# Kernel tuning notes

Measured on AMD Instinct MI355X. Metric: run time of the kernel, lower is better.

## Reference

```python
import jax, jax.numpy as jnp
import numpy as np

N = 60000   # cells
F = 256     # CELL_FEATURE_DIM
H = 128     # HIDDEN_DIM
NH = 8      # NUM_HEADS
DH = H // NH
L = 2       # NUM_LAYERS
C = 256     # tissue clusters
E = 600000  # cell edges
ET = 1500   # tissue edges
NCLS = 4


def _seg_softmax(s, seg, n):
    # numerically stable softmax within segments; s: [E, NH]
    m = jax.ops.segment_max(s, seg, num_segments=n)
    e = jnp.exp(s - m[seg])
    z = jax.ops.segment_sum(e, seg, num_segments=n)
    return e / z[seg]


def _forward(cell_features, cluster_labels, cell_edge_index, tissue_edge_index,
             W_cell_proj, b_cell_proj, W_tissue_proj, b_tissue_proj,
             gat_W, gat_asrc, gat_adst, gat_b, gcn_W, gcn_b,
             bu_Wq, bu_Wk, bu_Wv, bu_bq, bu_bk, bu_bv, bu_Wo, bu_bo,
             td_Wv, td_bv, td_Wo, td_bo,
             gru_Wih, gru_bih, gru_Whh, gru_bhh,
             Wc1, bc1, Wc2, bc2, Wc3, bc3):
    lab = cluster_labels
    # tissue node init = per-cluster mean of raw cell features (as in _construct_tissue_graph)
    cnt = jax.ops.segment_sum(jnp.ones((N,), jnp.float32), lab, num_segments=C)
    tissue_x = jax.ops.segment_sum(cell_features, lab, num_segments=C) / jnp.maximum(cnt, 1.0)[:, None]

    cell_h = cell_features @ W_cell_proj.T + b_cell_proj      # [N, H]
    tissue_h = tissue_x @ W_tissue_proj.T + b_tissue_proj     # [C, H]

    # add self-loops (PyG GATConv / GCNConv default)
    csrc = jnp.concatenate([cell_edge_index[0], jnp.arange(N, dtype=cell_edge_index.dtype)])
    cdst = jnp.concatenate([cell_edge_index[1], jnp.arange(N, dtype=cell_edge_index.dtype)])
    tsrc = jnp.concatenate([tissue_edge_index[0], jnp.arange(C, dtype=tissue_edge_index.dtype)])
    tdst = jnp.concatenate([tissue_edge_index[1], jnp.arange(C, dtype=tissue_edge_index.dtype)])

    # GCN symmetric norm (deg over col, PyG gcn_norm)
    degc = jax.ops.segment_sum(jnp.ones_like(tdst, dtype=jnp.float32), tdst, num_segments=C)
    dinv = jnp.where(degc > 0, 1.0 / jnp.sqrt(degc), 0.0)
    w_e = (dinv[tsrc] * dinv[tdst])[:, None]

    scale = 1.0 / jnp.sqrt(jnp.float32(DH))

    for l in range(L):
        # --- GATConv (multi-head concat) + ELU ---
        h = (cell_h @ gat_W[l].T).reshape(N, NH, DH)
        a_s = (h * gat_asrc[l]).sum(-1)  # [N, NH]
        a_d = (h * gat_adst[l]).sum(-1)
        e = jax.nn.leaky_relu(a_s[csrc] + a_d[cdst], negative_slope=0.2)  # [E+N, NH]
        alpha = _seg_softmax(e, cdst, N)
        agg = jax.ops.segment_sum(h[csrc] * alpha[:, :, None], cdst, num_segments=N)
        cell_h = jax.nn.elu(agg.reshape(N, H) + gat_b[l])

        # --- GCNConv + ReLU on tissue graph ---
        th = tissue_h @ gcn_W[l].T
        tissue_h = jax.nn.relu(jax.ops.segment_sum(th[tsrc] * w_e, tdst, num_segments=C) + gcn_b[l])

        # --- bottom-up cross-level attention: tissue queries attend over their cells ---
        q = ((tissue_h @ bu_Wq.T + bu_bq) * scale).reshape(C, NH, DH)
        k = (cell_h @ bu_Wk.T + bu_bk).reshape(N, NH, DH)
        v = (cell_h @ bu_Wv.T + bu_bv).reshape(N, NH, DH)
        s_att = (q[lab] * k).sum(-1)                       # [N, NH]
        al = _seg_softmax(s_att, lab, C)
        ctx = jax.ops.segment_sum(v * al[:, :, None], lab, num_segments=C).reshape(C, H)
        tissue_h = ctx @ bu_Wo.T + bu_bo

        # --- top-down attention: each cell attends to its single tissue node ---
        # softmax over one key is identically 1, so output = Wo(Wv t + bv) + bo gathered per cell
        td = (tissue_h @ td_Wv.T + td_bv) @ td_Wo.T + td_bo  # [C, H]
        cell_h = td[lab]

        # --- top-down GRUCell refinement: x=[cell;tissue], h=cell ---
        x_in = jnp.concatenate([cell_h, tissue_h[lab]], axis=-1)  # [N, 2H]
        gi = x_in @ gru_Wih.T + gru_bih
        gh = cell_h @ gru_Whh.T + gru_bhh
        r = jax.nn.sigmoid(gi[:, :H] + gh[:, :H])
        z = jax.nn.sigmoid(gi[:, H:2 * H] + gh[:, H:2 * H])
        n = jnp.tanh(gi[:, 2 * H:] + r * gh[:, 2 * H:])
        cell_h = (1.0 - z) * n + z * cell_h

    # dual-pooling readouts (single graph: batch all zeros)
    emb = jnp.concatenate([cell_h.mean(0), cell_h.max(0), tissue_h.mean(0), tissue_h.max(0)])[None, :]  # [1, 4H]
    h1 = jax.nn.relu(emb @ Wc1.T + bc1)
    h2 = jax.nn.relu(h1 @ Wc2.T + bc2)
    return h2 @ Wc3.T + bc3  # [1, NCLS]


def setup_inputs() -> dict:
    k = jax.random.split(jax.random.key(0), 40)
    s = 0.05
    r = lambda i, shape: jax.random.normal(k[i], shape, jnp.float32) * s
    return dict(
        cell_features=jax.random.normal(k[0], (N, F), jnp.float32),
        cell_edge_index=jax.random.randint(k[1], (2, E), 0, N),
        cluster_labels=jax.random.randint(k[2], (N,), 0, C),
        tissue_edge_index=jax.random.randint(k[3], (2, ET), 0, C),
        W_cell_proj=r(4, (H, F)), b_cell_proj=r(5, (H,)),
        W_tissue_proj=r(6, (H, F)), b_tissue_proj=r(7, (H,)),
        gat_W=r(8, (L, H, H)), gat_asrc=r(9, (L, NH, DH)), gat_adst=r(10, (L, NH, DH)), gat_b=r(11, (L, H)),
        gcn_W=r(12, (L, H, H)), gcn_b=r(13, (L, H)),
        bu_Wq=r(14, (H, H)), bu_Wk=r(15, (H, H)), bu_Wv=r(16, (H, H)),
        bu_bq=r(17, (H,)), bu_bk=r(18, (H,)), bu_bv=r(19, (H,)),
        bu_Wo=r(20, (H, H)), bu_bo=r(21, (H,)),
        td_Wv=r(22, (H, H)), td_bv=r(23, (H,)), td_Wo=r(24, (H, H)), td_bo=r(25, (H,)),
        gru_Wih=r(26, (3 * H, 2 * H)), gru_bih=r(27, (3 * H,)),
        gru_Whh=r(28, (3 * H, H)), gru_bhh=r(29, (3 * H,)),
        Wc1=r(30, (2 * H, 4 * H)), bc1=r(31, (2 * H,)),
        Wc2=r(32, (H, 2 * H)), bc2=r(33, (H,)),
        Wc3=r(34, (NCLS, H)), bc3=r(35, (NCLS,)),
    )


def reference(cell_features, cell_edge_index, cluster_labels, tissue_edge_index,
              W_cell_proj, b_cell_proj, W_tissue_proj, b_tissue_proj,
              gat_W, gat_asrc, gat_adst, gat_b, gcn_W, gcn_b,
              bu_Wq, bu_Wk, bu_Wv, bu_bq, bu_bk, bu_bv, bu_Wo, bu_bo,
              td_Wv, td_bv, td_Wo, td_bo,
              gru_Wih, gru_bih, gru_Whh, gru_bhh,
              Wc1, bc1, Wc2, bc2, Wc3, bc3):
    return _forward(cell_features, cluster_labels, cell_edge_index, tissue_edge_index,
                    W_cell_proj, b_cell_proj, W_tissue_proj, b_tissue_proj,
                    gat_W, gat_asrc, gat_adst, gat_b, gcn_W, gcn_b,
                    bu_Wq, bu_Wk, bu_Wv, bu_bq, bu_bk, bu_bv, bu_Wo, bu_bo,
                    td_Wv, td_bv, td_Wo, td_bo,
                    gru_Wih, gru_bih, gru_Whh, gru_bhh,
                    Wc1, bc1, Wc2, bc2, Wc3, bc3)
```

## Files before the change

### kernel.cpp

```cpp
#include <hip/hip_runtime.h>
#include <math.h>

constexpr int N  = 60000;
constexpr int F  = 256;
constexpr int H  = 128;
constexpr int C  = 256;
constexpr int E  = 600000;
constexpr int ET = 1500;
constexpr int NB = (N + 1023) / 1024;
constexpr int SPL = 8;
constexpr int PB  = 16;

typedef __attribute__((ext_vector_type(8))) short short8;
typedef __attribute__((ext_vector_type(4))) float f32x4;

__device__ __forceinline__ unsigned short f2b(float f) {
  unsigned int u = __float_as_uint(f);
  return (unsigned short)((u + 0x7FFFu + ((u >> 16) & 1u)) >> 16);
}
__device__ __forceinline__ float b2f(unsigned short b) {
  return __uint_as_float(((unsigned int)b) << 16);
}

__global__ void hg_hist(const int* __restrict__ cdst, int* __restrict__ deg,
                        const int* __restrict__ lab, int* __restrict__ ccnt) {
  int e = blockIdx.x * 256 + threadIdx.x;
  if (e < E) atomicAdd(&deg[cdst[e]], 1);
  if (e < N) atomicAdd(&ccnt[lab[e]], 1);
}

__global__ __launch_bounds__(256) void hg_scan1(const int* __restrict__ deg, int* __restrict__ off,
                                                int* __restrict__ btot, int n) {
  int b = blockIdx.x, t = threadIdx.x;
  int i0 = b * 1024 + t * 4;
  __shared__ int sums[256];
  int d0 = 0, d1 = 0, d2 = 0, d3 = 0;
  if (i0 + 3 < n) {
    int4 dd = *(const int4*)&deg[i0];
    d0 = dd.x; d1 = dd.y; d2 = dd.z; d3 = dd.w;
  } else {
    if (i0     < n) d0 = deg[i0];
    if (i0 + 1 < n) d1 = deg[i0 + 1];
    if (i0 + 2 < n) d2 = deg[i0 + 2];
    if (i0 + 3 < n) d3 = deg[i0 + 3];
  }
  int s = d0 + d1 + d2 + d3;
  sums[t] = s;
  __syncthreads();
  for (int ofs = 1; ofs < 256; ofs <<= 1) {
    int v = (t >= ofs) ? sums[t - ofs] : 0;
    __syncthreads();
    sums[t] += v;
    __syncthreads();
  }
  int excl = sums[t] - s;
  if (t == 255) btot[b] = sums[t];
  int run = excl;
  if (i0     < n) off[i0]     = run; run += d0;
  if (i0 + 1 < n) off[i0 + 1] = run; run += d1;
  if (i0 + 2 < n) off[i0 + 2] = run; run += d2;
  if (i0 + 3 < n) off[i0 + 3] = run;
}

__global__ __launch_bounds__(256) void hg_scan2_setup(int* __restrict__ btot, int* __restrict__ off,
                                                      const int* __restrict__ ccnt, int* __restrict__ coff,
                                                      const int* __restrict__ tsrc, const int* __restrict__ tdst,
                                                      int* __restrict__ toff, int* __restrict__ tlist,
                                                      float* __restrict__ dinv) {
  __shared__ int sa[256], sb[256], sc2[256];
  int t = threadIdx.x;
  if (blockIdx.x == 0) {
    if (t < 64) sa[t] = (t < NB) ? btot[t] : 0;
    __syncthreads();
    if (t == 0) {
      int r = 0;
      for (int i = 0; i < NB; ++i) { int v = sa[i]; sa[i] = r; r += v; }
      off[N] = r;
    }
    __syncthreads();
    if (t < NB) btot[t] = sa[t];
  } else if (blockIdx.x == 1) {
    int v0 = ccnt[t];
    sa[t] = v0;
    __syncthreads();
    for (int ofs = 1; ofs < 256; ofs <<= 1) {
      int v = (t >= ofs) ? sa[t - ofs] : 0;
      __syncthreads();
      sa[t] += v;
      __syncthreads();
    }
    coff[t + 1] = sa[t];
    if (t == 0) coff[0] = 0;
  } else {
    sa[t] = 0;
    __syncthreads();
    for (int e = t; e < ET; e += 256) atomicAdd(&sa[tdst[e]], 1);
    __syncthreads();
    int v = sa[t];
    dinv[t] = rsqrtf((float)(v + 1));
    sb[t] = v;
    __syncthreads();
    for (int ofs = 1; ofs < 256; ofs <<= 1) {
      int u = (t >= ofs) ? sb[t - ofs] : 0;
      __syncthreads();
      sb[t] += u;
      __syncthreads();
    }
    toff[t + 1] = sb[t];
    if (t == 0) toff[0] = 0;
    sc2[t] = sb[t] - v;
    __syncthreads();
    for (int e = t; e < ET; e += 256) {
      int d = tdst[e];
      int p = atomicAdd(&sc2[d], 1);
      tlist[p] = tsrc[e];
    }
  }
}

__global__ void hg_scan3(int* __restrict__ off, const int* __restrict__ btot, int n) {
  int b = blockIdx.x;
  int addv = btot[b];
  int i0 = b * 1024 + threadIdx.x * 4;
#pragma unroll
  for (int r = 0; r < 4; ++r)
    if (i0 + r < n) off[i0 + r] += addv;
}

__global__ void hg_scatter(const int* __restrict__ csrc, const int* __restrict__ cdst,
                           const int* __restrict__ off, int* __restrict__ cur, int* __restrict__ csr,
                           const int* __restrict__ lab, const int* __restrict__ coff,
                           int* __restrict__ ccur, int* __restrict__ list) {
  int e = blockIdx.x * 256 + threadIdx.x;
  if (e < E) {
    int d = cdst[e];
    int p = atomicAdd(&cur[d], 1);
    csr[off[d] + p] = csrc[e];
  }
  if (e < N) {
    int c = lab[e];
    int p = atomicAdd(&ccur[c], 1);
    list[coff[c] + p] = e;
  }
}

struct TJob { const float* src; float* dst; int SR; int SC; int dld; };
struct PrepArgs {
  TJob j[8];
  const float* gatW1; const float* Wcp; const float* bcp; short* Wcompb; float* bcomp;
  const float* tdWo; const float* tdWv; const float* tdbv; const float* tdbo;
  float* A_td; float* Wcat_t; float* bcat;
};

__global__ __launch_bounds__(256) void hg_prep1(PrepArgs a) {
  int y = blockIdx.y, t = threadIdx.x;
  if (y < 8) {
    TJob jb = a.j[y];
    int total = jb.SR * jb.SC;
    for (int idx = blockIdx.x * 256 + t; idx < total; idx += gridDim.x * 256) {
      int r = idx / jb.SC, c = idx - r * jb.SC;
      jb.dst[(size_t)c * jb.dld + r] = jb.src[idx];
    }
  } else if (y == 8) {
    int j = blockIdx.x, k = t;
    float acc = 0.f;
#pragma unroll 4
    for (int m = 0; m < 128; ++m) acc = fmaf(a.gatW1[j * 128 + m], a.Wcp[m * 256 + k], acc);
    a.Wcompb[(size_t)j * 256 + k] = (short)f2b(acc);
    if (k == 0) {
      float b = 0.f;
      for (int m = 0; m < 128; ++m) b = fmaf(a.gatW1[j * 128 + m], a.bcp[m], b);
      a.bcomp[j] = b;
    }
  } else if (blockIdx.x < 64) {
    int j = blockIdx.x * 2 + (t >> 7), k = t & 127;
    float acc = 0.f;
#pragma unroll 4
    for (int p = 0; p < 128; ++p) acc = fmaf(a.tdWo[j * 128 + p], a.tdWv[p * 128 + k], acc);
    a.A_td[j * 128 + k] = acc;
    a.Wcat_t[k * 896 + j] = acc;
    if (k == 0) {
      float b = 0.f;
      for (int p = 0; p < 128; ++p) b = fmaf(a.tdWo[j * 128 + p], a.tdbv[p], b);
      a.bcat[j] = b + a.tdbo[j];
    }
  }
}

__global__ __launch_bounds__(256) void hg_pc2b(const float* __restrict__ Wih, const float* __restrict__ bih,
                                               const float* __restrict__ Whh, const float* __restrict__ bhh,
                                               const float* __restrict__ A_td, float* __restrict__ Wcat_t,
                                               float* __restrict__ bcat) {
  int jj = blockIdx.x * 2 + (threadIdx.x >> 7), k = threadIdx.x & 127;
  const float* coef;
  float extra, bb;
  int dcol, j;
  if (jj < 384) {
    j = jj; coef = Wih + (size_t)j * 256; extra = Wih[(size_t)j * 256 + 128 + k]; dcol = 128 + j; bb = bih[j];
  } else {
    j = jj - 384; coef = Whh + (size_t)j * 128; extra = 0.f; dcol = 512 + j; bb = bhh[j];
  }
  float a = 0.f;
#pragma unroll 4
  for (int m = 0; m < 128; ++m) a = fmaf(coef[m], A_td[m * 128 + k], a);
  Wcat_t[k * 896 + dcol] = a + extra;
  if (k == 0) {
    float b = 0.f;
    for (int m = 0; m < 128; ++m) b = fmaf(coef[m], bcat[m], b);
    bcat[dcol] = b + bb;
  }
}

__global__ __launch_bounds__(256, 2) void hg_gemm_coef(
    const float* __restrict__ A, int M, int rtiles,
    const short* __restrict__ Wb,
    const float* __restrict__ bias,
    unsigned short* __restrict__ outp,
    const float* __restrict__ avs, const float* __restrict__ avd,
    float* __restrict__ o_s, float* __restrict__ o_d,
    const int* __restrict__ list, const int* __restrict__ coff,
    const float* __restrict__ Wtpt, const float* __restrict__ btp, float* __restrict__ tish) {
  __shared__ float mrow[256];
  const int t = threadIdx.x;

  if (blockIdx.x >= rtiles) {
    int c = blockIdx.x - rtiles;
    int s0 = coff[c], n = coff[c + 1] - s0;
    float acc = 0.f;
#pragma unroll 4
    for (int i = 0; i < n; ++i) acc += A[(size_t)list[s0 + i] * F + t];
    mrow[t] = acc / fmaxf((float)n, 1.f);
    __syncthreads();
    if (t < 128) {
      float a = btp[t];
#pragma unroll 4
      for (int k = 0; k < 256; ++k) a = fmaf(mrow[k], Wtpt[k * 128 + t], a);
      tish[c * 128 + t] = a;
    }
    return;
  }

  const int w = t >> 6, l = t & 63;
  const int li = l & 15, lk = l >> 4;
  const int m0 = blockIdx.x * 128 + w * 32;

  f32x4 zero = {0.f, 0.f, 0.f, 0.f};
  f32x4 acc[2][8];
#pragma unroll
  for (int rt = 0; rt < 2; ++rt)
#pragma unroll
    for (int ct = 0; ct < 8; ++ct) acc[rt][ct] = zero;

  const int r0 = m0 + li, r1 = m0 + 16 + li;
  const bool v0 = r0 < M, v1 = r1 < M;
  const float* a0p = A + (size_t)r0 * 256 + lk * 8;
  const float* a1p = A + (size_t)r1 * 256 + lk * 8;

  for (int kc = 0; kc < 256; kc += 32) {
    short8 bf[8];
#pragma unroll
    for (int ct = 0; ct < 8; ++ct)
      bf[ct] = *(const short8*)&Wb[(size_t)(ct * 16 + li) * 256 + kc + lk * 8];
    short8 af0 = {0, 0, 0, 0, 0, 0, 0, 0};
    short8 af1 = {0, 0, 0, 0, 0, 0, 0, 0};
    if (v0) {
      float4 x = *(const float4*)(a0p + kc);
      float4 y = *(const float4*)(a0p + kc + 4);
      af0[0] = (short)f2b(x.x); af0[1] = (short)f2b(x.y); af0[2] = (short)f2b(x.z); af0[3] = (short)f2b(x.w);
      af0[4] = (short)f2b(y.x); af0[5] = (short)f2b(y.y); af0[6] = (short)f2b(y.z); af0[7] = (short)f2b(y.w);
    }
    if (v1) {
      float4 x = *(const float4*)(a1p + kc);
      float4 y = *(const float4*)(a1p + kc + 4);
      af1[0] = (short)f2b(x.x); af1[1] = (short)f2b(x.y); af1[2] = (short)f2b(x.z); af1[3] = (short)f2b(x.w);
      af1[4] = (short)f2b(y.x); af1[5] = (short)f2b(y.y); af1[6] = (short)f2b(y.z); af1[7] = (short)f2b(y.w);
    }
#pragma unroll
    for (int ct = 0; ct < 8; ++ct) {
      acc[0][ct] = __builtin_amdgcn_mfma_f32_16x16x32_bf16(af0, bf[ct], acc[0][ct], 0, 0, 0);
      acc[1][ct] = __builtin_amdgcn_mfma_f32_16x16x32_bf16(af1, bf[ct], acc[1][ct], 0, 0, 0);
    }
  }

#pragma unroll
  for (int ct = 0; ct < 8; ++ct) {
    float bj = bias[ct * 16 + li];
    float as = avs[ct * 16 + li];
    float ad = avd[ct * 16 + li];
#pragma unroll
    for (int rt = 0; rt < 2; ++rt) {
#pragma unroll
      for (int r = 0; r < 4; ++r) {
        int gm = m0 + rt * 16 + lk * 4 + r;
        float v = acc[rt][ct][r] + bj;
        if (gm < M) outp[(size_t)gm * 128 + ct * 16 + li] = f2b(v);
        float ps = v * as, pd = v * ad;
        ps += __shfl_xor(ps, 1); ps += __shfl_xor(ps, 2); ps += __shfl_xor(ps, 4); ps += __shfl_xor(ps, 8);
        pd += __shfl_xor(pd, 1); pd += __shfl_xor(pd, 2); pd += __shfl_xor(pd, 4); pd += __shfl_xor(pd, 8);
        if (li == 0 && gm < M) {
          o_s[(size_t)gm * 8 + ct] = ps;
          o_d[(size_t)gm * 8 + ct] = pd;
        }
      }
    }
  }
}

#define GMAXE 64
__global__ __launch_bounds__(256) void hg_gat_agg(
    const unsigned short* __restrict__ hproj, const float* __restrict__ a_s,
    const float* __restrict__ a_d, const int* __restrict__ remap,
    const int* __restrict__ off, const int* __restrict__ csr,
    const float* __restrict__ bias, unsigned short* __restrict__ outh,
    const float* __restrict__ qk, const float* __restrict__ qb,
    const int* __restrict__ lab, const int* __restrict__ nodelist,
    float* __restrict__ satt, int nNodes) {
  const int wid = threadIdx.x >> 6;
  const int l = threadIdx.x & 63;
  const int gid = blockIdx.x * 4 + wid;
  __shared__ int srcs_s[4][GMAXE];
  __shared__ float w_s[4][GMAXE][8];
  if (gid >= nNodes) return;
  const int node = nodelist[gid];
  int* srcs = srcs_s[wid];
  float (*wls)[8] = w_s[wid];
  const int o0 = off[node], deg = off[node + 1] - o0;
  const int cl = lab[node];
  const int dl = remap ? cl : node;
  const int hsc = l & 7;
  const int q4 = l & 31;
  const int sub = l >> 5;
  const int hq = q4 >> 2;
  const float adh = a_d[dl * 8 + hsc];
  const float ash = a_s[dl * 8 + hsc];
  float msc = -INFINITY, zsc = 0.f;
  float4 acc = make_float4(0.f, 0.f, 0.f, 0.f);
  const ushort4* hp4 = (const ushort4*)hproj;

  for (int cb = 0; cb < deg; cb += GMAXE) {
    const int len = min(GMAXE, deg - cb);
    if (l < len) {
      int s = csr[o0 + cb + l];
      srcs[l] = remap ? remap[s] : s;
    }
    asm volatile("s_waitcnt lgkmcnt(0)" ::: "memory");
    float lm = -INFINITY;
    for (int base = 0; base < len; base += 8) {
      int e = base + (l >> 3);
      if (e < len) {
        float sc = a_s[srcs[e] * 8 + hsc] + adh;
        sc = sc > 0.f ? sc : 0.2f * sc;
        wls[e][hsc] = sc;
        lm = fmaxf(lm, sc);
      }
    }
    lm = fmaxf(lm, __shfl_xor(lm, 8));
    lm = fmaxf(lm, __shfl_xor(lm, 16));
    lm = fmaxf(lm, __shfl_xor(lm, 32));
    float mnew = fmaxf(msc, lm);
    float rs = __expf(msc - mnew);
    float zc = 0.f;
    asm volatile("s_waitcnt lgkmcnt(0)" ::: "memory");
    for (int base = 0; base < len; base += 8) {
      int e = base + (l >> 3);
      if (e < len) {
        float wv = __expf(wls[e][hsc] - mnew);
        wls[e][hsc] = wv;
        zc += wv;
      }
    }
    asm volatile("s_waitcnt lgkmcnt(0)" ::: "memory");
    zc += __shfl_xor(zc, 8); zc += __shfl_xor(zc, 16); zc += __shfl_xor(zc, 32);
    zsc = zsc * rs + zc;
    msc = mnew;
    float rsa = __shfl(rs, hq);
    acc.x *= rsa; acc.y *= rsa; acc.z *= rsa; acc.w *= rsa;
    for (int e = sub; e < len; e += 2) {
      float wv = wls[e][hq];
      ushort4 hv = hp4[(size_t)srcs[e] * 32 + q4];
      acc.x = fmaf(wv, b2f(hv.x), acc.x);
      acc.y = fmaf(wv, b2f(hv.y), acc.y);
      acc.z = fmaf(wv, b2f(hv.z), acc.z);
      acc.w = fmaf(wv, b2f(hv.w), acc.w);
    }
  }
  float ssl = ash + adh;
  ssl = ssl > 0.f ? ssl : 0.2f * ssl;
  float mnew = fmaxf(msc, ssl);
  float rs = __expf(msc - mnew);
  float wsl = __expf(ssl - mnew);
  zsc = zsc * rs + wsl;
  float rsa = __shfl(rs, hq);
  float wsa = __shfl(wsl, hq);
  float zh = __shfl(zsc, hq);
  acc.x *= rsa; acc.y *= rsa; acc.z *= rsa; acc.w *= rsa;
  acc.x += __shfl_xor(acc.x, 32);
  acc.y += __shfl_xor(acc.y, 32);
  acc.z += __shfl_xor(acc.z, 32);
  acc.w += __shfl_xor(acc.w, 32);
  ushort4 hvs = hp4[(size_t)dl * 32 + q4];
  acc.x = fmaf(wsa, b2f(hvs.x), acc.x);
  acc.y = fmaf(wsa, b2f(hvs.y), acc.y);
  acc.z = fmaf(wsa, b2f(hvs.z), acc.z);
  acc.w = fmaf(wsa, b2f(hvs.w), acc.w);
  float inv = 1.f / zh;
  float4 bv4 = *(const float4*)&bias[q4 * 4];
  float4 o;
  o.x = acc.x * inv + bv4.x;
  o.y = acc.y * inv + bv4.y;
  o.z = acc.z * inv + bv4.z;
  o.w = acc.w * inv + bv4.w;
  o.x = o.x > 0.f ? o.x : __expf(o.x) - 1.f;
  o.y = o.y > 0.f ? o.y : __expf(o.y) - 1.f;
  o.z = o.z > 0.f ? o.z : __expf(o.z) - 1.f;
  o.w = o.w > 0.f ? o.w : __expf(o.w) - 1.f;
  if (sub == 0) {
    ushort4 ov = make_ushort4(f2b(o.x), f2b(o.y), f2b(o.z), f2b(o.w));
    ((ushort4*)outh)[(size_t)node * 32 + q4] = ov;
  }

  const float4* qk4 = (const float4*)(qk + (size_t)cl * 1024);
  float p0, p1, p2, p3;
  {
    float4 qv0 = qk4[(sub * 4 + 0) * 32 + q4];
    float4 qv1 = qk4[(sub * 4 + 1) * 32 + q4];
    float4 qv2 = qk4[(sub * 4 + 2) * 32 + q4];
    float4 qv3 = qk4[(sub * 4 + 3) * 32 + q4];
    p0 = o.x * qv0.x + o.y * qv0.y + o.z * qv0.z + o.w * qv0.w;
    p1 = o.x * qv1.x + o.y * qv1.y + o.z * qv1.z + o.w * qv1.w;
    p2 = o.x * qv2.x + o.y * qv2.y + o.z * qv2.z + o.w * qv2.w;
    p3 = o.x * qv3.x + o.y * qv3.y + o.z * qv3.z + o.w * qv3.w;
  }
  int b4f = (l >> 4) & 1, b3f = (l >> 3) & 1;
  float snd0 = b4f ? p0 : p2, snd1 = b4f ? p1 : p3;
  float kp0  = b4f ? p2 : p0, kp1  = b4f ? p3 : p1;
  kp0 += __shfl_xor(snd0, 16);
  kp1 += __shfl_xor(snd1, 16);
  float snd = b3f ? kp0 : kp1;
  float kp  = b3f ? kp1 : kp0;
  kp += __shfl_xor(snd, 8);
  kp += __shfl_xor(kp, 4);
  kp += __shfl_xor(kp, 2);
  kp += __shfl_xor(kp, 1);
  int h = sub * 4 + b4f * 2 + b3f;
  if ((l & 7) == 0) satt[(size_t)node * 8 + h] = kp + qb[cl * 8 + h];
}

__global__ __launch_bounds__(128) void hg_gcn_q(const float* __restrict__ tin, const int* __restrict__ toff,
                                                const int* __restrict__ tlist, const float* __restrict__ dinv,
                                                const float* __restrict__ gt, const float* __restrict__ gcnb,
                                                const float* __restrict__ Wqt, const float* __restrict__ bq,
                                                const float* __restrict__ Wk, const float* __restrict__ bk,
                                                float* __restrict__ qk, float* __restrict__ qb) {
  int c = blockIdx.x, t = threadIdx.x;
  __shared__ float xa[128], trow[128], qrow[128];
  float dc = dinv[c];
  float acc = tin[c * 128 + t] * dc * dc;
  int s0 = toff[c], s1 = toff[c + 1];
  for (int i = s0; i < s1; ++i) {
    int s = tlist[i];
    acc = fmaf(tin[s * 128 + t], dinv[s] * dc, acc);
  }
  xa[t] = acc;
  __syncthreads();
  float th = 0.f;
#pragma unroll 4
  for (int k = 0; k < 128; ++k) th = fmaf(xa[k], gt[k * 128 + t], th);
  float vv = fmaxf(th + gcnb[t], 0.f);
  trow[t] = vv;
  __syncthreads();
  float qa = bq[t];
#pragma unroll 4
  for (int k = 0; k < 128; ++k) qa = fmaf(trow[k], Wqt[k * 128 + t], qa);
  qrow[t] = qa * 0.25f;
  __syncthreads();
#pragma unroll
  for (int h = 0; h < 8; ++h) {
    float s = 0.f;
#pragma unroll
    for (int j = 0; j < 16; ++j) s = fmaf(Wk[(size_t)(h * 16 + j) * 128 + t], qrow[h * 16 + j], s);
    qk[((size_t)c * 8 + h) * 128 + t] = s;
  }
  if (t < 8) {
    float s = 0.f;
#pragma unroll
    for (int j = 0; j < 16; ++j) s = fmaf(qrow[t * 16 + j], bk[t * 16 + j], s);
    qb[c * 8 + t] = s;
  }
}

__global__ __launch_bounds__(256) void hg_bu_part(
    const float* __restrict__ s_att, const unsigned short* __restrict__ hcell,
    const int* __restrict__ list, const int* __restrict__ coff,
    float* __restrict__ pm, float* __restrict__ pz, float* __restrict__ pmacc) {
  int c = blockIdx.x, sp = blockIdx.y, t = threadIdx.x;
  int s0 = coff[c], n = coff[c + 1] - s0;
  int chunk = (n + SPL - 1) / SPL;
  int b0 = min(n, sp * chunk), b1 = min(n, b0 + chunk);
  int cnt = b1 - b0;
  int tf = t & 127, half = t >> 7;
  __shared__ float red[32][8];
  __shared__ float mh[8];
  __shared__ int cells[64];
  __shared__ float wl[64][8];
  __shared__ float msh[8][128];
  int g = t >> 3, h8 = t & 7;
  float lm = -INFINITY;
  for (int i = g; i < cnt; i += 32) lm = fmaxf(lm, s_att[(size_t)list[s0 + b0 + i] * 8 + h8]);
  red[g][h8] = lm;
  __syncthreads();
  if (t < 8) {
    float m2 = -INFINITY;
#pragma unroll
    for (int i = 0; i < 32; ++i) m2 = fmaxf(m2, red[i][t]);
    mh[t] = m2;
  }
  __syncthreads();
  const float mloc = mh[t & 7];
  float zp = 0.f;
  float macc[8] = {0.f, 0.f, 0.f, 0.f, 0.f, 0.f, 0.f, 0.f};
  for (int cb = 0; cb < cnt; cb += 64) {
    int len = min(64, cnt - cb);
    if (t < len) cells[t] = list[s0 + b0 + cb + t];
    __syncthreads();
#pragma unroll
    for (int p = 0; p < 2; ++p) {
      int e = p * 32 + (t >> 3);
      if (e < len) {
        float w = __expf(s_att[(size_t)cells[e] * 8 + (t & 7)] - mloc);
        wl[e][t & 7] = w;
        zp += w;
      }
    }
    __syncthreads();
    for (int e = half; e < len; e += 2) {
      float x = b2f(hcell[(size_t)cells[e] * 128 + tf]);
      float4 w0 = *(const float4*)&wl[e][0];
      float4 w1 = *(const float4*)&wl[e][4];
      macc[0] = fmaf(w0.x, x, macc[0]);
      macc[1] = fmaf(w0.y, x, macc[1]);
      macc[2] = fmaf(w0.z, x, macc[2]);
      macc[3] = fmaf(w0.w, x, macc[3]);
      macc[4] = fmaf(w1.x, x, macc[4]);
      macc[5] = fmaf(w1.y, x, macc[5]);
      macc[6] = fmaf(w1.z, x, macc[6]);
      macc[7] = fmaf(w1.w, x, macc[7]);
    }
    __syncthreads();
  }
  red[t >> 3][t & 7] = zp;
  __syncthreads();
  int pidx = (c * SPL + sp) * 8;
  if (t < 8) {
    float z = 0.f;
#pragma unroll
    for (int i = 0; i < 32; ++i) z += red[i][t];
    pz[pidx + t] = z;
    pm[pidx + t] = mh[t];
  }
  if (half) {
#pragma unroll
    for (int h = 0; h < 8; ++h) msh[h][tf] = macc[h];
  }
  __syncthreads();
  if (!half) {
#pragma unroll
    for (int h = 0; h < 8; ++h) pmacc[(size_t)(pidx + h) * 128 + tf] = macc[h] + msh[h][tf];
  }
}

__global__ __launch_bounds__(256) void hg_bu_chain(
    const float* __restrict__ pm, const float* __restrict__ pz, const float* __restrict__ pmacc,
    const float* __restrict__ Wv, const float* __restrict__ bv,
    const float* __restrict__ Wot, const float* __restrict__ bo,
    const float* __restrict__ Wcat_t, const float* __restrict__ bcat,
    const float* __restrict__ gatWt, const float* __restrict__ avs, const float* __restrict__ avd,
    float* __restrict__ tish, float* __restrict__ ccell,
    unsigned short* __restrict__ hprojc, float* __restrict__ a_s2, float* __restrict__ a_d2) {
  int c = blockIdx.x, t = threadIdx.x;
  int tf = t & 127, half = t >> 7;
  __shared__ float mh[8], zh[8];
  __shared__ float sscale[SPL][8];
  __shared__ float msh[8][128];
  __shared__ float b0[128], b1[128], part[2][128], catv[896];
  const int pbase = c * SPL * 8;
  if (t < 8) {
    float mg = -INFINITY;
#pragma unroll
    for (int s = 0; s < SPL; ++s) mg = fmaxf(mg, pm[pbase + s * 8 + t]);
    mh[t] = mg;
  }
  __syncthreads();
  if (t < SPL * 8) {
    int s = t >> 3, h = t & 7;
    float ms = pm[pbase + s * 8 + h];
    sscale[s][h] = (ms > -1e37f) ? __expf(ms - mh[h]) : 0.f;
  }
  __syncthreads();
  if (t < 8) {
    float z = 0.f;
#pragma unroll
    for (int s = 0; s < SPL; ++s) z += pz[pbase + s * 8 + t] * sscale[s][t];
    zh[t] = (z > 0.f) ? 1.f / z : 0.f;
  }
  __syncthreads();
#pragma unroll
  for (int hh = 0; hh < 4; ++hh) {
    int h = half * 4 + hh;
    float a = 0.f;
#pragma unroll
    for (int s = 0; s < SPL; ++s)
      a = fmaf(pmacc[(size_t)(pbase + s * 8 + h) * 128 + tf], sscale[s][h], a);
    msh[h][tf] = a * zh[h];
  }
  __syncthreads();
  {
    int h = tf >> 4;
    float ps = 0.f;
    const float* wp = Wv + (size_t)tf * 128 + half * 64;
    const float* mp = &msh[h][half * 64];
#pragma unroll 4
    for (int k = 0; k < 64; ++k) ps = fmaf(wp[k], mp[k], ps);
    part[half][tf] = ps;
  }
  __syncthreads();
  if (t < 128) b0[t] = part[0][t] + part[1][t] + bv[t];
  __syncthreads();
  int ks = half;
  {
    float ps = 0.f;
    const float* wp = Wot + (size_t)ks * 64 * 128 + tf;
#pragma unroll 4
    for (int k = 0; k < 64; ++k) ps = fmaf(b0[ks * 64 + k], wp[k * 128], ps);
    part[ks][tf] = ps;
  }
  __syncthreads();
  if (t < 128) {
    float vv = part[0][t] + part[1][t] + bo[t];
    b1[t] = vv;
    tish[c * 128 + t] = vv;
  }
  __syncthreads();
  for (int j = t; j < 896; j += 256) {
    float a = bcat[j];
#pragma unroll 4
    for (int k = 0; k < 128; ++k) a = fmaf(b1[k], Wcat_t[k * 896 + j], a);
    catv[j] = a;
  }
  __syncthreads();
  if (t < 128) {
    float td = catv[t];
    float r = 1.f / (1.f + expf(-(catv[128 + t] + catv[512 + t])));
    float zz = 1.f / (1.f + expf(-(catv[256 + t] + catv[640 + t])));
    float nn = tanhf(catv[384 + t] + r * catv[768 + t]);
    float cn = (1.f - zz) * nn + zz * td;
    ccell[c * 128 + t] = cn;
    b0[t] = cn;
  }
  __syncthreads();
  if (gatWt) {
    float ps = 0.f;
    const float* wp = gatWt + (size_t)ks * 64 * 128 + tf;
#pragma unroll 4
    for (int k = 0; k < 64; ++k) ps = fmaf(b0[ks * 64 + k], wp[k * 128], ps);
    part[ks][tf] = ps;
    __syncthreads();
    if (t < 128) {
      float hp = part[0][t] + part[1][t];
      hprojc[c * 128 + t] = f2b(hp);
      float pss = hp * avs[t], pdd = hp * avd[t];
      pss += __shfl_xor(pss, 1); pss += __shfl_xor(pss, 2); pss += __shfl_xor(pss, 4); pss += __shfl_xor(pss, 8);
      pdd += __shfl_xor(pdd, 1); pdd += __shfl_xor(pdd, 2); pdd += __shfl_xor(pdd, 4); pdd += __shfl_xor(pdd, 8);
      if ((t & 15) == 0) {
        a_s2[c * 8 + (t >> 4)] = pss;
        a_d2[c * 8 + (t >> 4)] = pdd;
      }
    }
  }
}

__global__ __launch_bounds__(256) void hg_pool(const float* __restrict__ ccell2, const float* __restrict__ tish,
                                               const int* __restrict__ cnt, float* __restrict__ part) {
  int b = blockIdx.x, t = threadIdx.x;
  int c0 = b * (C / PB);
  if (t < 128) {
    float sm = 0.f, mx = -INFINITY;
#pragma unroll 4
    for (int i = 0; i < C / PB; ++i) {
      int c = c0 + i;
      float vv = ccell2[c * 128 + t];
      int n = cnt[c];
      sm += (float)n * vv;
      if (n > 0) mx = fmaxf(mx, vv);
    }
    part[b * 512 + t] = sm;
    part[b * 512 + 128 + t] = mx;
  } else {
    int tt = t - 128;
    float sm = 0.f, mx = -INFINITY;
#pragma unroll 4
    for (int i = 0; i < C / PB; ++i) {
      int c = c0 + i;
      float vv = tish[c * 128 + tt];
      sm += vv;
      mx = fmaxf(mx, vv);
    }
    part[b * 512 + 256 + tt] = sm;
    part[b * 512 + 384 + tt] = mx;
  }
}

__global__ __launch_bounds__(256) void hg_mlp(const float* __restrict__ part, const float* __restrict__ Wc1t,
                                              const float* __restrict__ bc1, const float* __restrict__ Wc2t,
                                              const float* __restrict__ bc2, const float* __restrict__ Wc3,
                                              const float* __restrict__ bc3, float* __restrict__ outp) {
  __shared__ float emb[512], h1s[256], h2s[128];
  int t = threadIdx.x;
  if (t < 128) {
    float sm = 0.f, mx = -INFINITY;
#pragma unroll
    for (int b = 0; b < PB; ++b) {
      sm += part[b * 512 + t];
      mx = fmaxf(mx, part[b * 512 + 128 + t]);
    }
    emb[t] = sm / (float)N;
    emb[128 + t] = mx;
  } else {
    int tt = t - 128;
    float sm = 0.f, mx = -INFINITY;
#pragma unroll
    for (int b = 0; b < PB; ++b) {
      sm += part[b * 512 + 256 + tt];
      mx = fmaxf(mx, part[b * 512 + 384 + tt]);
    }
    emb[256 + tt] = sm * (1.f / (float)C);
    emb[384 + tt] = mx;
  }
  __syncthreads();
  float a = bc1[t];
#pragma unroll 4
  for (int kk = 0; kk < 512; ++kk) a = fmaf(emb[kk], Wc1t[kk * 256 + t], a);
  h1s[t] = fmaxf(a, 0.f);
  __syncthreads();
  if (t < 128) {
    float a2 = bc2[t];
#pragma unroll 4
    for (int kk = 0; kk < 256; ++kk) a2 = fmaf(h1s[kk], Wc2t[kk * 128 + t], a2);
    h2s[t] = fmaxf(a2, 0.f);
  }
  __syncthreads();
  if (t < 4) {
    float o = bc3[t];
    for (int kk = 0; kk < 128; ++kk) o = fmaf(h2s[kk], Wc3[t * 128 + kk], o);
    outp[t] = o;
  }
}

extern "C" void kernel_launch(void* const* d_in, const int* in_sizes, int n_in,
                              void* d_out, int out_size, void* d_ws, size_t ws_size,
                              hipStream_t stream) {
  (void)in_sizes; (void)n_in; (void)out_size; (void)ws_size;
  const float* feat  = (const float*)d_in[0];
  const int*   eidx  = (const int*)d_in[1];
  const int*   lab   = (const int*)d_in[2];
  const int*   tidx  = (const int*)d_in[3];
  const float* Wcp   = (const float*)d_in[4];
  const float* bcp   = (const float*)d_in[5];
  const float* Wtp   = (const float*)d_in[6];
  const float* btp   = (const float*)d_in[7];
  const float* gatW  = (const float*)d_in[8];
  const float* gasrc = (const float*)d_in[9];
  const float* gadst = (const float*)d_in[10];
  const float* gatb  = (const float*)d_in[11];
  const float* gcnW  = (const float*)d_in[12];
  const float* gcnb  = (const float*)d_in[13];
  const float* buWq  = (const float*)d_in[14];
  const float* buWk  = (const float*)d_in[15];
  const float* buWv  = (const float*)d_in[16];
  const float* bubq  = (const float*)d_in[17];
  const float* bubk  = (const float*)d_in[18];
  const float* bubv  = (const float*)d_in[19];
  const float* buWo  = (const float*)d_in[20];
  const float* bubo  = (const float*)d_in[21];
  const float* tdWv  = (const float*)d_in[22];
  const float* tdbv  = (const float*)d_in[23];
  const float* tdWo  = (const float*)d_in[24];
  const float* tdbo  = (const float*)d_in[25];
  const float* Wih   = (const float*)d_in[26];
  const float* bih   = (const float*)d_in[27];
  const float* Whh   = (const float*)d_in[28];
  const float* bhh   = (const float*)d_in[29];
  const float* Wc1   = (const float*)d_in[30];
  const float* bc1   = (const float*)d_in[31];
  const float* Wc2   = (const float*)d_in[32];
  const float* bc2   = (const float*)d_in[33];
  const float* Wc3   = (const float*)d_in[34];
  const float* bc3   = (const float*)d_in[35];
  float* outp = (float*)d_out;

  const int* csrc = eidx;
  const int* cdst = eidx + E;
  const int* tsrc = tidx;
  const int* tdst = tidx + ET;

  char* w = (char*)d_ws;
  auto alloc = [&](size_t bytes) -> void* {
    void* p = (void*)w;
    w += (bytes + 255) & ~(size_t)255;
    return p;
  };
  char* cnt0 = w;
  int* deg_cell = (int*)alloc((size_t)N * 4);
  int* cur_cell = (int*)alloc((size_t)N * 4);
  int* clu_cnt  = (int*)alloc((size_t)C * 4);
  int* clu_cur  = (int*)alloc((size_t)C * 4);
  size_t cntBytes = (size_t)(w - cnt0);
  int* off_cell = (int*)alloc((size_t)(N + 1) * 4);
  int* btot     = (int*)alloc(64 * 4);
  int* csr      = (int*)alloc((size_t)E * 4);
  int* clu_off  = (int*)alloc((size_t)(C + 1) * 4);
  int* clu_list = (int*)alloc((size_t)N * 4);
  int* toff     = (int*)alloc((size_t)(C + 1) * 4);
  int* tlist    = (int*)alloc((size_t)ET * 4);
  float* dinv   = (float*)alloc((size_t)C * 4);
  unsigned short* buf1 = (unsigned short*)alloc((size_t)N * 128 * 2);
  unsigned short* buf2 = (unsigned short*)alloc((size_t)N * 128 * 2);
  float* a_s    = (float*)alloc((size_t)N * 8 * 4);
  float* a_d    = (float*)alloc((size_t)N * 8 * 4);
  float* s_att  = (float*)alloc((size_t)N * 8 * 4);
  float* tish   = (float*)alloc((size_t)C * 128 * 4);
  float* qkb    = (float*)alloc((size_t)C * 8 * 128 * 4);
  float* qbb    = (float*)alloc((size_t)C * 8 * 4);
  float* ccell  = (float*)alloc((size_t)C * 128 * 4);
  unsigned short* hprojc = (unsigned short*)alloc((size_t)C * 128 * 2);
  float* a_sc   = (float*)alloc((size_t)C * 8 * 4);
  float* a_dc   = (float*)alloc((size_t)C * 8 * 4);
  float* pm     = (float*)alloc((size_t)C * SPL * 8 * 4);
  float* pz     = (float*)alloc((size_t)C * SPL * 8 * 4);
  float* pmacc  = (float*)alloc((size_t)C * SPL * 8 * 128 * 4);
  float* poolp  = (float*)alloc((size_t)PB * 512 * 4);
  float* A_td   = (float*)alloc(128 * 128 * 4);
  float* Wcat_t = (float*)alloc(128 * 896 * 4);
  float* bcat   = (float*)alloc(896 * 4);
  short* Wcompb = (short*)alloc(128 * 256 * 2);
  float* bcomp  = (float*)alloc(128 * 4);
  float* Wtpt   = (float*)alloc(256 * 128 * 4);
  float* g1t    = (float*)alloc(128 * 128 * 4);
  float* g2t    = (float*)alloc(128 * 128 * 4);
  float* Wqt    = (float*)alloc(128 * 128 * 4);
  float* Wot    = (float*)alloc(128 * 128 * 4);
  float* gatW2t = (float*)alloc(128 * 128 * 4);
  float* Wc1t   = (float*)alloc(512 * 256 * 4);
  float* Wc2t   = (float*)alloc(256 * 128 * 4);

  hipMemsetAsync(cnt0, 0, cntBytes, stream);

  hg_hist<<<(E + 255) / 256, 256, 0, stream>>>(cdst, deg_cell, lab, clu_cnt);
  hg_scan1<<<NB, 256, 0, stream>>>(deg_cell, off_cell, btot, N);
  hg_scan2_setup<<<3, 256, 0, stream>>>(btot, off_cell, clu_cnt, clu_off, tsrc, tdst, toff, tlist, dinv);
  hg_scan3<<<NB, 256, 0, stream>>>(off_cell, btot, N);
  hg_scatter<<<(E + 255) / 256, 256, 0, stream>>>(csrc, cdst, off_cell, cur_cell, csr,
                                                  lab, clu_off, clu_cur, clu_list);

  PrepArgs pa;
  pa.j[0] = {Wtp,            Wtpt,   128, 256, 128};
  pa.j[1] = {gcnW,           g1t,    128, 128, 128};
  pa.j[2] = {gcnW + 128*128, g2t,    128, 128, 128};
  pa.j[3] = {buWq,           Wqt,    128, 128, 128};
  pa.j[4] = {buWo,           Wot,    128, 128, 128};
  pa.j[5] = {gatW + 128*128, gatW2t, 128, 128, 128};
  pa.j[6] = {Wc1,            Wc1t,   256, 512, 256};
  pa.j[7] = {Wc2,            Wc2t,   128, 256, 128};
  pa.gatW1 = gatW; pa.Wcp = Wcp; pa.bcp = bcp; pa.Wcompb = Wcompb; pa.bcomp = bcomp;
  pa.tdWo = tdWo; pa.tdWv = tdWv; pa.tdbv = tdbv; pa.tdbo = tdbo;
  pa.A_td = A_td; pa.Wcat_t = Wcat_t; pa.bcat = bcat;
  hg_prep1<<<dim3(128, 10), 256, 0, stream>>>(pa);
  hg_pc2b<<<384, 256, 0, stream>>>(Wih, bih, Whh, bhh, A_td, Wcat_t, bcat);

  const int RT = (N + 127) / 128;
  hg_gemm_coef<<<RT + C, 256, 0, stream>>>(feat, N, RT, Wcompb, bcomp, buf2, gasrc, gadst, a_s, a_d,
                                           clu_list, clu_off, Wtpt, btp, tish);
  hg_gcn_q<<<C, 128, 0, stream>>>(tish, toff, tlist, dinv, g1t, gcnb, Wqt, bubq, buWk, bubk, qkb, qbb);
  hg_gat_agg<<<(N + 3) / 4, 256, 0, stream>>>(buf2, a_s, a_d, nullptr, off_cell, csr, gatb, buf1,
                                              qkb, qbb, lab, clu_list, s_att, N);
  hg_bu_part<<<dim3(C, SPL), 256, 0, stream>>>(s_att, buf1, clu_list, clu_off, pm, pz, pmacc);
  hg_bu_chain<<<C, 256, 0, stream>>>(pm, pz, pmacc, buWv, bubv, Wot, bubo, Wcat_t, bcat,
                                     gatW2t, gasrc + 128, gadst + 128, tish, ccell, hprojc, a_sc, a_dc);
  hg_gcn_q<<<C, 128, 0, stream>>>(tish, toff, tlist, dinv, g2t, gcnb + 128, Wqt, bubq, buWk, bubk, qkb, qbb);
  hg_gat_agg<<<(N + 3) / 4, 256, 0, stream>>>(hprojc, a_sc, a_dc, lab, off_cell, csr, gatb + 128, buf1,
                                              qkb, qbb, lab, clu_list, s_att, N);
  hg_bu_part<<<dim3(C, SPL), 256, 0, stream>>>(s_att, buf1, clu_list, clu_off, pm, pz, pmacc);
  hg_bu_chain<<<C, 256, 0, stream>>>(pm, pz, pmacc, buWv, bubv, Wot, bubo, Wcat_t, bcat,
                                     nullptr, nullptr, nullptr, tish, ccell, nullptr, nullptr, nullptr);

  hg_pool<<<PB, 256, 0, stream>>>(ccell, tish, clu_cnt, poolp);
  hg_mlp<<<1, 256, 0, stream>>>(poolp, Wc1t, bc1, Wc2t, bc2, Wc3, bc3, outp);
}
```

Measured before the change: 546.0 us.

## Fold GAT attention vectors into GEMM weights and tabulate layer-2 cluster attention

```diff
diff --git a/kernel.cpp b/kernel.cpp
--- a/kernel.cpp
+++ b/kernel.cpp
@@ -150,6 +150,7 @@
   const float* gatW1; const float* Wcp; const float* bcp; short* Wcompb; float* bcomp;
   const float* tdWo; const float* tdWv; const float* tdbv; const float* tdbo;
   float* A_td; float* Wcat_t; float* bcat;
+  const float* avs; const float* avd; float* sbias;
 };
 
 __global__ __launch_bounds__(256) void hg_prep1(PrepArgs a) {
@@ -172,7 +173,8 @@
       for (int m = 0; m < 128; ++m) b = fmaf(a.gatW1[j * 128 + m], a.bcp[m], b);
       a.bcomp[j] = b;
     }
-  } else if (blockIdx.x < 64) {
+  } else if (y == 9) {
+    if (blockIdx.x >= 64) return;
     int j = blockIdx.x * 2 + (t >> 7), k = t & 127;
     float acc = 0.f;
 #pragma unroll 4
@@ -183,6 +185,27 @@
       float b = 0.f;
       for (int p = 0; p < 128; ++p) b = fmaf(a.tdWo[j * 128 + p], a.tdbv[p], b);
       a.bcat[j] = b + a.tdbo[j];
+    }
+  } else {
+    if (blockIdx.x >= 16) return;
+    __shared__ float u[128];
+    int dir = blockIdx.x >> 3, h = blockIdx.x & 7;
+    const float* av = (dir == 0 ? a.avs : a.avd) + h * 16;
+    if (t < 128) {
+      float s = 0.f;
+#pragma unroll
+      for (int j = 0; j < 16; ++j) s = fmaf(a.gatW1[(size_t)(h * 16 + j) * 128 + t], av[j], s);
+      u[t] = s;
+    }
+    __syncthreads();
+    float q = 0.f;
+#pragma unroll 4
+    for (int m = 0; m < 128; ++m) q = fmaf(u[m], a.Wcp[m * 256 + t], q);
+    a.Wcompb[(size_t)(128 + dir * 8 + h) * 256 + t] = (short)f2b(q);
+    if (t == 0) {
+      float cs = 0.f;
+      for (int m = 0; m < 128; ++m) cs = fmaf(u[m], a.bcp[m], cs);
+      a.sbias[dir * 8 + h] = cs;
     }
   }
 }
@@ -211,13 +234,13 @@
   }
 }
 
-__global__ __launch_bounds__(256, 2) void hg_gemm_coef(
+__global__ __launch_bounds__(256, 3) void hg_gemm_coef(
     const float* __restrict__ A, int M, int rtiles,
     const short* __restrict__ Wb,
     const float* __restrict__ bias,
+    const float* __restrict__ sbias,
     unsigned short* __restrict__ outp,
-    const float* __restrict__ avs, const float* __restrict__ avd,
-    float* __restrict__ o_s, float* __restrict__ o_d,
+    float* __restrict__ ab,
     const int* __restrict__ list, const int* __restrict__ coff,
     const float* __restrict__ Wtpt, const float* __restrict__ btp, float* __restrict__ tish) {
   __shared__ float mrow[256];
@@ -245,11 +268,11 @@
   const int m0 = blockIdx.x * 128 + w * 32;
 
   f32x4 zero = {0.f, 0.f, 0.f, 0.f};
-  f32x4 acc[2][8];
+  f32x4 acc[2][9];
 #pragma unroll
   for (int rt = 0; rt < 2; ++rt)
 #pragma unroll
-    for (int ct = 0; ct < 8; ++ct) acc[rt][ct] = zero;
+    for (int ct = 0; ct < 9; ++ct) acc[rt][ct] = zero;
 
   const int r0 = m0 + li, r1 = m0 + 16 + li;
   const bool v0 = r0 < M, v1 = r1 < M;
@@ -257,9 +280,9 @@
   const float* a1p = A + (size_t)r1 * 256 + lk * 8;
 
   for (int kc = 0; kc < 256; kc += 32) {
-    short8 bf[8];
-#pragma unroll
-    for (int ct = 0; ct < 8; ++ct)
+    short8 bf[9];
+#pragma unroll
+    for (int ct = 0; ct < 9; ++ct)
       bf[ct] = *(const short8*)&Wb[(size_t)(ct * 16 + li) * 256 + kc + lk * 8];
     short8 af0 = {0, 0, 0, 0, 0, 0, 0, 0};
     short8 af1 = {0, 0, 0, 0, 0, 0, 0, 0};
@@ -276,7 +299,7 @@
       af1[4] = (short)f2b(y.x); af1[5] = (short)f2b(y.y); af1[6] = (short)f2b(y.z); af1[7] = (short)f2b(y.w);
     }
 #pragma unroll
-    for (int ct = 0; ct < 8; ++ct) {
+    for (int ct = 0; ct < 9; ++ct) {
       acc[0][ct] = __builtin_amdgcn_mfma_f32_16x16x32_bf16(af0, bf[ct], acc[0][ct], 0, 0, 0);
       acc[1][ct] = __builtin_amdgcn_mfma_f32_16x16x32_bf16(af1, bf[ct], acc[1][ct], 0, 0, 0);
     }
@@ -285,22 +308,23 @@
 #pragma unroll
   for (int ct = 0; ct < 8; ++ct) {
     float bj = bias[ct * 16 + li];
-    float as = avs[ct * 16 + li];
-    float ad = avd[ct * 16 + li];
 #pragma unroll
     for (int rt = 0; rt < 2; ++rt) {
 #pragma unroll
       for (int r = 0; r < 4; ++r) {
         int gm = m0 + rt * 16 + lk * 4 + r;
-        float v = acc[rt][ct][r] + bj;
-        if (gm < M) outp[(size_t)gm * 128 + ct * 16 + li] = f2b(v);
-        float ps = v * as, pd = v * ad;
-        ps += __shfl_xor(ps, 1); ps += __shfl_xor(ps, 2); ps += __shfl_xor(ps, 4); ps += __shfl_xor(ps, 8);
-        pd += __shfl_xor(pd, 1); pd += __shfl_xor(pd, 2); pd += __shfl_xor(pd, 4); pd += __shfl_xor(pd, 8);
-        if (li == 0 && gm < M) {
-          o_s[(size_t)gm * 8 + ct] = ps;
-          o_d[(size_t)gm * 8 + ct] = pd;
-        }
+        if (gm < M) outp[(size_t)gm * 128 + ct * 16 + li] = f2b(acc[rt][ct][r] + bj);
+      }
+    }
+  }
+  {
+    float sb = sbias[li];
+#pragma unroll
+    for (int rt = 0; rt < 2; ++rt) {
+#pragma unroll
+      for (int r = 0; r < 4; ++r) {
+        int gm = m0 + rt * 16 + lk * 4 + r;
+        if (gm < M) ab[(size_t)gm * 16 + li] = acc[rt][8][r] + sb;
       }
     }
   }
@@ -308,8 +332,7 @@
 
 #define GMAXE 64
 __global__ __launch_bounds__(256) void hg_gat_agg(
-    const unsigned short* __restrict__ hproj, const float* __restrict__ a_s,
-    const float* __restrict__ a_d, const int* __restrict__ remap,
+    const unsigned short* __restrict__ hproj, const float* __restrict__ ab,
     const int* __restrict__ off, const int* __restrict__ csr,
     const float* __restrict__ bias, unsigned short* __restrict__ outh,
     const float* __restrict__ qk, const float* __restrict__ qb,
@@ -326,29 +349,25 @@
   float (*wls)[8] = w_s[wid];
   const int o0 = off[node], deg = off[node + 1] - o0;
   const int cl = lab[node];
-  const int dl = remap ? cl : node;
   const int hsc = l & 7;
   const int q4 = l & 31;
   const int sub = l >> 5;
   const int hq = q4 >> 2;
-  const float adh = a_d[dl * 8 + hsc];
-  const float ash = a_s[dl * 8 + hsc];
+  const float adh = ab[(size_t)node * 16 + 8 + hsc];
+  const float ash = ab[(size_t)node * 16 + hsc];
   float msc = -INFINITY, zsc = 0.f;
   float4 acc = make_float4(0.f, 0.f, 0.f, 0.f);
   const ushort4* hp4 = (const ushort4*)hproj;
 
   for (int cb = 0; cb < deg; cb += GMAXE) {
     const int len = min(GMAXE, deg - cb);
-    if (l < len) {
-      int s = csr[o0 + cb + l];
-      srcs[l] = remap ? remap[s] : s;
-    }
+    if (l < len) srcs[l] = csr[o0 + cb + l];
     asm volatile("s_waitcnt lgkmcnt(0)" ::: "memory");
     float lm = -INFINITY;
     for (int base = 0; base < len; base += 8) {
       int e = base + (l >> 3);
       if (e < len) {
-        float sc = a_s[srcs[e] * 8 + hsc] + adh;
+        float sc = ab[(size_t)srcs[e] * 16 + hsc] + adh;
         sc = sc > 0.f ? sc : 0.2f * sc;
         wls[e][hsc] = sc;
         lm = fmaxf(lm, sc);
@@ -398,7 +417,7 @@
   acc.y += __shfl_xor(acc.y, 32);
   acc.z += __shfl_xor(acc.z, 32);
   acc.w += __shfl_xor(acc.w, 32);
-  ushort4 hvs = hp4[(size_t)dl * 32 + q4];
+  ushort4 hvs = hp4[(size_t)node * 32 + q4];
   acc.x = fmaf(wsa, b2f(hvs.x), acc.x);
   acc.y = fmaf(wsa, b2f(hvs.y), acc.y);
   acc.z = fmaf(wsa, b2f(hvs.z), acc.z);
@@ -444,6 +463,129 @@
   kp += __shfl_xor(kp, 1);
   int h = sub * 4 + b4f * 2 + b3f;
   if ((l & 7) == 0) satt[(size_t)node * 8 + h] = kp + qb[cl * 8 + h];
+}
+
+__global__ __launch_bounds__(256) void hg_ttab(const float* __restrict__ a_sc, const float* __restrict__ a_dc,
+                                               float* __restrict__ T) {
+  int cd = blockIdx.x, cs = threadIdx.x;
+  __shared__ float as[256][8];
+  __shared__ float mx[8];
+#pragma unroll
+  for (int h = 0; h < 8; ++h) as[cs][h] = a_sc[cs * 8 + h];
+  __syncthreads();
+  if (cs < 8) {
+    float m = -INFINITY;
+    for (int i = 0; i < 256; ++i) m = fmaxf(m, as[i][cs]);
+    mx[cs] = m;
+  }
+  __syncthreads();
+  float* Trow = T + ((size_t)cd * 256 + cs) * 8;
+#pragma unroll
+  for (int h = 0; h < 8; ++h) {
+    float ad = a_dc[cd * 8 + h];
+    float s = as[cs][h] + ad;
+    s = s > 0.f ? s : 0.2f * s;
+    float sm = mx[h] + ad;
+    sm = sm > 0.f ? sm : 0.2f * sm;
+    Trow[h] = __expf(s - sm);
+  }
+}
+
+__global__ __launch_bounds__(256) void hg_gat_agg2(
+    const unsigned short* __restrict__ hproj,
+    const float* __restrict__ T,
+    const int* __restrict__ lab, const int* __restrict__ off, const int* __restrict__ csr,
+    const float* __restrict__ bias, unsigned short* __restrict__ outh,
+    const float* __restrict__ qk, const float* __restrict__ qb,
+    const int* __restrict__ nodelist, float* __restrict__ satt, int nNodes) {
+  const int wid = threadIdx.x >> 6;
+  const int l = threadIdx.x & 63;
+  const int gid = blockIdx.x * 4 + wid;
+  __shared__ int srcs_s[4][GMAXE];
+  if (gid >= nNodes) return;
+  const int node = nodelist[gid];
+  int* srcs = srcs_s[wid];
+  const int o0 = off[node], deg = off[node + 1] - o0;
+  const int cd = lab[node];
+  const int q4 = l & 31;
+  const int sub = l >> 5;
+  const int hq = q4 >> 2;
+  const float* Trow = T + (size_t)cd * 2048;
+  const ushort4* hp4 = (const ushort4*)hproj;
+  float4 acc = make_float4(0.f, 0.f, 0.f, 0.f);
+  float z = 0.f;
+
+  for (int cb = 0; cb < deg; cb += GMAXE) {
+    const int len = min(GMAXE, deg - cb);
+    if (l < len) srcs[l] = lab[csr[o0 + cb + l]];
+    asm volatile("s_waitcnt lgkmcnt(0)" ::: "memory");
+    for (int e = sub; e < len; e += 2) {
+      int cs = srcs[e];
+      float tw = Trow[cs * 8 + hq];
+      ushort4 hv = hp4[(size_t)cs * 32 + q4];
+      acc.x = fmaf(tw, b2f(hv.x), acc.x);
+      acc.y = fmaf(tw, b2f(hv.y), acc.y);
+      acc.z = fmaf(tw, b2f(hv.z), acc.z);
+      acc.w = fmaf(tw, b2f(hv.w), acc.w);
+      z += tw;
+    }
+    asm volatile("s_waitcnt lgkmcnt(0)" ::: "memory");
+  }
+  acc.x += __shfl_xor(acc.x, 32);
+  acc.y += __shfl_xor(acc.y, 32);
+  acc.z += __shfl_xor(acc.z, 32);
+  acc.w += __shfl_xor(acc.w, 32);
+  z += __shfl_xor(z, 32);
+  {
+    float tw = Trow[cd * 8 + hq];
+    ushort4 hv = hp4[(size_t)cd * 32 + q4];
+    acc.x = fmaf(tw, b2f(hv.x), acc.x);
+    acc.y = fmaf(tw, b2f(hv.y), acc.y);
+    acc.z = fmaf(tw, b2f(hv.z), acc.z);
+    acc.w = fmaf(tw, b2f(hv.w), acc.w);
+    z += tw;
+  }
+  float inv = 1.f / z;
+  float4 bv4 = *(const float4*)&bias[q4 * 4];
+  float4 o;
+  o.x = acc.x * inv + bv4.x;
+  o.y = acc.y * inv + bv4.y;
+  o.z = acc.z * inv + bv4.z;
+  o.w = acc.w * inv + bv4.w;
+  o.x = o.x > 0.f ? o.x : __expf(o.x) - 1.f;
+  o.y = o.y > 0.f ? o.y : __expf(o.y) - 1.f;
+  o.z = o.z > 0.f ? o.z : __expf(o.z) - 1.f;
+  o.w = o.w > 0.f ? o.w : __expf(o.w) - 1.f;
+  if (sub == 0) {
+    ushort4 ov = make_ushort4(f2b(o.x), f2b(o.y), f2b(o.z), f2b(o.w));
+    ((ushort4*)outh)[(size_t)node * 32 + q4] = ov;
+  }
+
+  const float4* qk4 = (const float4*)(qk + (size_t)cd * 1024);
+  float p0, p1, p2, p3;
+  {
+    float4 qv0 = qk4[(sub * 4 + 0) * 32 + q4];
+    float4 qv1 = qk4[(sub * 4 + 1) * 32 + q4];
+    float4 qv2 = qk4[(sub * 4 + 2) * 32 + q4];
+    float4 qv3 = qk4[(sub * 4 + 3) * 32 + q4];
+    p0 = o.x * qv0.x + o.y * qv0.y + o.z * qv0.z + o.w * qv0.w;
+    p1 = o.x * qv1.x + o.y * qv1.y + o.z * qv1.z + o.w * qv1.w;
+    p2 = o.x * qv2.x + o.y * qv2.y + o.z * qv2.z + o.w * qv2.w;
+    p3 = o.x * qv3.x + o.y * qv3.y + o.z * qv3.z + o.w * qv3.w;
+  }
+  int b4f = (l >> 4) & 1, b3f = (l >> 3) & 1;
+  float snd0 = b4f ? p0 : p2, snd1 = b4f ? p1 : p3;
+  float kp0  = b4f ? p2 : p0, kp1  = b4f ? p3 : p1;
+  kp0 += __shfl_xor(snd0, 16);
+  kp1 += __shfl_xor(snd1, 16);
+  float snd = b3f ? kp0 : kp1;
+  float kp  = b3f ? kp1 : kp0;
+  kp += __shfl_xor(snd, 8);
+  kp += __shfl_xor(kp, 4);
+  kp += __shfl_xor(kp, 2);
+  kp += __shfl_xor(kp, 1);
+  int h = sub * 4 + b4f * 2 + b3f;
+  if ((l & 7) == 0) satt[(size_t)node * 8 + h] = kp + qb[cd * 8 + h];
 }
 
 __global__ __launch_bounds__(128) void hg_gcn_q(const float* __restrict__ tin, const int* __restrict__ toff,
@@ -825,8 +967,7 @@
   float* dinv   = (float*)alloc((size_t)C * 4);
   unsigned short* buf1 = (unsigned short*)alloc((size_t)N * 128 * 2);
   unsigned short* buf2 = (unsigned short*)alloc((size_t)N * 128 * 2);
-  float* a_s    = (float*)alloc((size_t)N * 8 * 4);
-  float* a_d    = (float*)alloc((size_t)N * 8 * 4);
+  float* ab     = (float*)alloc((size_t)N * 16 * 4);
   float* s_att  = (float*)alloc((size_t)N * 8 * 4);
   float* tish   = (float*)alloc((size_t)C * 128 * 4);
   float* qkb    = (float*)alloc((size_t)C * 8 * 128 * 4);
@@ -835,6 +976,7 @@
   unsigned short* hprojc = (unsigned short*)alloc((size_t)C * 128 * 2);
   float* a_sc   = (float*)alloc((size_t)C * 8 * 4);
   float* a_dc   = (float*)alloc((size_t)C * 8 * 4);
+  float* Ttab   = (float*)alloc((size_t)C * 256 * 8 * 4);
   float* pm     = (float*)alloc((size_t)C * SPL * 8 * 4);
   float* pz     = (float*)alloc((size_t)C * SPL * 8 * 4);
   float* pmacc  = (float*)alloc((size_t)C * SPL * 8 * 128 * 4);
@@ -842,8 +984,9 @@
   float* A_td   = (float*)alloc(128 * 128 * 4);
   float* Wcat_t = (float*)alloc(128 * 896 * 4);
   float* bcat   = (float*)alloc(896 * 4);
-  short* Wcompb = (short*)alloc(128 * 256 * 2);
+  short* Wcompb = (short*)alloc(144 * 256 * 2);
   float* bcomp  = (float*)alloc(128 * 4);
+  float* sbias  = (float*)alloc(16 * 4);
   float* Wtpt   = (float*)alloc(256 * 128 * 4);
   float* g1t    = (float*)alloc(128 * 128 * 4);
   float* g2t    = (float*)alloc(128 * 128 * 4);
@@ -874,21 +1017,23 @@
   pa.gatW1 = gatW; pa.Wcp = Wcp; pa.bcp = bcp; pa.Wcompb = Wcompb; pa.bcomp = bcomp;
   pa.tdWo = tdWo; pa.tdWv = tdWv; pa.tdbv = tdbv; pa.tdbo = tdbo;
   pa.A_td = A_td; pa.Wcat_t = Wcat_t; pa.bcat = bcat;
-  hg_prep1<<<dim3(128, 10), 256, 0, stream>>>(pa);
+  pa.avs = gasrc; pa.avd = gadst; pa.sbias = sbias;
+  hg_prep1<<<dim3(128, 11), 256, 0, stream>>>(pa);
   hg_pc2b<<<384, 256, 0, stream>>>(Wih, bih, Whh, bhh, A_td, Wcat_t, bcat);
 
   const int RT = (N + 127) / 128;
-  hg_gemm_coef<<<RT + C, 256, 0, stream>>>(feat, N, RT, Wcompb, bcomp, buf2, gasrc, gadst, a_s, a_d,
+  hg_gemm_coef<<<RT + C, 256, 0, stream>>>(feat, N, RT, Wcompb, bcomp, sbias, buf2, ab,
                                            clu_list, clu_off, Wtpt, btp, tish);
   hg_gcn_q<<<C, 128, 0, stream>>>(tish, toff, tlist, dinv, g1t, gcnb, Wqt, bubq, buWk, bubk, qkb, qbb);
-  hg_gat_agg<<<(N + 3) / 4, 256, 0, stream>>>(buf2, a_s, a_d, nullptr, off_cell, csr, gatb, buf1,
+  hg_gat_agg<<<(N + 3) / 4, 256, 0, stream>>>(buf2, ab, off_cell, csr, gatb, buf1,
                                               qkb, qbb, lab, clu_list, s_att, N);
   hg_bu_part<<<dim3(C, SPL), 256, 0, stream>>>(s_att, buf1, clu_list, clu_off, pm, pz, pmacc);
   hg_bu_chain<<<C, 256, 0, stream>>>(pm, pz, pmacc, buWv, bubv, Wot, bubo, Wcat_t, bcat,
                                      gatW2t, gasrc + 128, gadst + 128, tish, ccell, hprojc, a_sc, a_dc);
   hg_gcn_q<<<C, 128, 0, stream>>>(tish, toff, tlist, dinv, g2t, gcnb + 128, Wqt, bubq, buWk, bubk, qkb, qbb);
-  hg_gat_agg<<<(N + 3) / 4, 256, 0, stream>>>(hprojc, a_sc, a_dc, lab, off_cell, csr, gatb + 128, buf1,
-                                              qkb, qbb, lab, clu_list, s_att, N);
+  hg_ttab<<<C, 256, 0, stream>>>(a_sc, a_dc, Ttab);
+  hg_gat_agg2<<<(N + 3) / 4, 256, 0, stream>>>(hprojc, Ttab, lab, off_cell, csr, gatb + 128, buf1,
+                                               qkb, qbb, clu_list, s_att, N);
   hg_bu_part<<<dim3(C, SPL), 256, 0, stream>>>(s_att, buf1, clu_list, clu_off, pm, pz, pmacc);
   hg_bu_chain<<<C, 256, 0, stream>>>(pm, pz, pmacc, buWv, bubv, Wot, bubo, Wcat_t, bcat,
                                      nullptr, nullptr, nullptr, tish, ccell, nullptr, nullptr, nullptr);
```

New measurement: 557.4 us. +2.1%, slower.
